# Performance work log

Measured on AMD Instinct MI355X. Metric: run time of the kernel, lower is better.

Reference implementation:

```python
import jax, jax.numpy as jnp
import numpy as np
from jax import lax

VOCAB = 32000
D_MODEL = 1024
N_LAYERS = 4
D_STATE = 8
D_CONV = 4
EXPAND = 2
D_INNER = EXPAND * D_MODEL          # 2048
DT_RANK = (D_MODEL + 15) // 16      # 64
B, L = 2, 1024


def setup_inputs() -> dict:
    key = jax.random.key(0)
    ks = jax.random.split(key, 20)
    s = 0.02
    inp = {
        "input_ids": jax.random.randint(ks[0], (B, L), 0, VOCAB, dtype=jnp.int32),
        "embed": jax.random.normal(ks[1], (VOCAB, D_MODEL), jnp.float32) * s,
        "in_proj_w": jax.random.normal(ks[2], (N_LAYERS, 2 * D_INNER, D_MODEL), jnp.float32) * s,
        "conv_w": jax.random.normal(ks[3], (N_LAYERS, D_INNER, 1, D_CONV), jnp.float32) * s,
        "conv_b": jnp.zeros((N_LAYERS, D_INNER), jnp.float32),
        "x_proj_w": jax.random.normal(ks[4], (N_LAYERS, DT_RANK + 2 * D_STATE, D_INNER), jnp.float32) * s,
        "dt_proj_w": jax.random.normal(ks[5], (N_LAYERS, D_INNER, DT_RANK), jnp.float32) * s,
        "dt_proj_b": jax.random.normal(ks[6], (N_LAYERS, D_INNER), jnp.float32) * 0.1,
        "A_log": jnp.broadcast_to(jnp.log(jnp.arange(1, D_STATE + 1, dtype=jnp.float32)),
                                  (N_LAYERS, D_INNER, D_STATE)) + 0.0,
        "D": jnp.ones((N_LAYERS, D_INNER), jnp.float32),
        "out_proj_w": jax.random.normal(ks[7], (N_LAYERS, D_MODEL, D_INNER), jnp.float32) * s,
        "ln_g": jnp.ones((N_LAYERS, D_MODEL), jnp.float32),
        "ln_b": jnp.zeros((N_LAYERS, D_MODEL), jnp.float32),
        "fn_g": jnp.ones((D_MODEL,), jnp.float32),
        "fn_b": jnp.zeros((D_MODEL,), jnp.float32),
        "fc_w": jax.random.normal(ks[8], (VOCAB, D_MODEL), jnp.float32) * s,
        "fc_b": jnp.zeros((VOCAB,), jnp.float32),
    }
    return inp


def layer_norm(x, g, b, eps=1e-5):
    mu = jnp.mean(x, -1, keepdims=True)
    var = jnp.var(x, -1, keepdims=True)
    return (x - mu) * lax.rsqrt(var + eps) * g + b


def silu(x):
    return x * jax.nn.sigmoid(x)


def selective_scan(deltaA, deltaBu, C):
    # deltaA, deltaBu: (b,l,d,n); C: (b,l,n) -> y: (b,l,d)
    def step(h, inp):
        dA, dBu, c = inp
        h = dA * h + dBu                       # (b,d,n)
        y = jnp.einsum('bdn,bn->bd', h, c)
        return h, y
    h0 = jnp.zeros(deltaA.shape[:1] + deltaA.shape[2:], deltaA.dtype)
    _, ys = lax.scan(step, h0, (deltaA.transpose(1, 0, 2, 3),
                                deltaBu.transpose(1, 0, 2, 3),
                                C.transpose(1, 0, 2)))
    return ys.transpose(1, 0, 2)


def mamba_block(x, in_proj_w, conv_w, conv_b, x_proj_w, dt_proj_w, dt_proj_b, A_log, D, out_proj_w):
    # x: (b,l,d_model)
    xz = jnp.einsum('bld,ed->ble', x, in_proj_w)          # (b,l,2*di)
    xc, z = jnp.split(xz, 2, axis=-1)
    # causal depthwise conv1d, kernel D_CONV
    xc_ncl = xc.transpose(0, 2, 1)                         # (b,di,l)
    xc_ncl = lax.conv_general_dilated(
        xc_ncl, conv_w, window_strides=(1,), padding=[(D_CONV - 1, 0)],
        feature_group_count=D_INNER, dimension_numbers=('NCH', 'OIH', 'NCH'))
    xc = silu(xc_ncl.transpose(0, 2, 1) + conv_b)          # (b,l,di)
    x_dbl = jnp.einsum('bld,ed->ble', xc, x_proj_w)        # (b,l,dt_rank+2n)
    dt, Bm, Cm = jnp.split(x_dbl, [DT_RANK, DT_RANK + D_STATE], axis=-1)
    dt = jax.nn.softplus(jnp.einsum('blr,dr->bld', dt, dt_proj_w) + dt_proj_b)  # (b,l,di)
    A = -jnp.exp(A_log)                                    # (di,n)
    deltaA = jnp.exp(dt[..., None] * A)                    # (b,l,di,n)
    deltaBu = dt[..., None] * Bm[:, :, None, :] * xc[..., None]
    y = selective_scan(deltaA, deltaBu, Cm)                # (b,l,di)
    y = y + xc * D
    y = y * silu(z)
    return jnp.einsum('ble,de->bld', y, out_proj_w)


def reference(input_ids, embed, in_proj_w, conv_w, conv_b, x_proj_w, dt_proj_w,
              dt_proj_b, A_log, D, out_proj_w, ln_g, ln_b, fn_g, fn_b, fc_w, fc_b):
    x = embed[input_ids]                                   # (b,l,d)
    for i in range(N_LAYERS):
        out = mamba_block(x, in_proj_w[i], conv_w[i], conv_b[i], x_proj_w[i],
                          dt_proj_w[i], dt_proj_b[i], A_log[i], D[i], out_proj_w[i])
        x = layer_norm(out + x, ln_g[i], ln_b[i])
    x = layer_norm(x, fn_g, fn_b)
    logits = jnp.einsum('bld,vd->blv', x, fc_w) + fc_b
    return logits
```

## Files before the change

### kernel.cpp

```cpp
#include <hip/hip_runtime.h>
#include <cstddef>
#include <cstdint>

#define D_MODEL 1024
#define D_INNER 2048
#define DT_RANK 64
#define D_STATE 8
#define NLAYERS 4
#define BATCH 2
#define SEQ 1024
#define M_ROWS (BATCH*SEQ)
#define VOCAB 32000
#define XPAD 128
#define NC 32
#define LC 32
#define XSK 8

typedef __attribute__((ext_vector_type(8))) short short8;
typedef __attribute__((ext_vector_type(4))) float f32x4;

#define GPTR(p) (const __attribute__((address_space(1))) void*)(p)
#define LPTR(p) (__attribute__((address_space(3))) void*)(p)

__device__ __forceinline__ float sigmoidf_(float x) { return 1.f / (1.f + __expf(-x)); }

__device__ __forceinline__ unsigned short f2bf(float f) {
    unsigned u = __float_as_uint(f);
    u += 0x7fffu + ((u >> 16) & 1u);
    return (unsigned short)(u >> 16);
}

__global__ __launch_bounds__(256) void cast_kernel(const float* __restrict__ in,
                                                   unsigned short* __restrict__ out, int n4)
{
    int i = blockIdx.x * 256 + threadIdx.x;
    if (i >= n4) return;
    float4 v = ((const float4*)in)[i];
    ushort4 o;
    o.x = f2bf(v.x); o.y = f2bf(v.y); o.z = f2bf(v.z); o.w = f2bf(v.w);
    ((ushort4*)out)[i] = o;
}

__global__ __launch_bounds__(256) void cast_pad_xproj(const float* __restrict__ in,
                                                      unsigned short* __restrict__ out)
{
    int i = blockIdx.x * 256 + threadIdx.x;
    if (i >= NLAYERS * XPAD * D_INNER / 4) return;
    int col4 = i & (D_INNER / 4 - 1);
    int row = (i >> 9) & (XPAD - 1);
    int layer = i >> 16;
    ushort4 o = {0, 0, 0, 0};
    if (row < 80) {
        float4 v = ((const float4*)(in + ((size_t)layer * 80 + row) * D_INNER))[col4];
        o.x = f2bf(v.x); o.y = f2bf(v.y); o.z = f2bf(v.z); o.w = f2bf(v.w);
    }
    ((ushort4*)out)[i] = o;
}

__global__ __launch_bounds__(256) void gather_kernel(const int* __restrict__ ids,
                                                     const float* __restrict__ embed,
                                                     float* __restrict__ x,
                                                     unsigned short* __restrict__ xb)
{
    int m = blockIdx.x;
    int t = threadIdx.x;
    int id = ids[m];
    float4 v = ((const float4*)(embed + (size_t)id * D_MODEL))[t];
    ((float4*)(x + (size_t)m * D_MODEL))[t] = v;
    ushort4 o;
    o.x = f2bf(v.x); o.y = f2bf(v.y); o.z = f2bf(v.z); o.w = f2bf(v.w);
    ((ushort4*)(xb + (size_t)m * D_MODEL))[t] = o;
}

template<int EPI>
__global__ __launch_bounds__(256) void gemm_bf16_nt(const unsigned short* __restrict__ A, int lda,
                                                    const unsigned short* __restrict__ B, int ldb,
                                                    float* __restrict__ C, int ldc,
                                                    int K, const float* __restrict__ bias)
{
    __shared__ unsigned short As[2][128 * 32];
    __shared__ unsigned short Bs[2][128 * 32];
    const int tid = threadIdx.x;

    const int gm = gridDim.x;
    const int bid = blockIdx.y * gm + blockIdx.x;
    const int q = (gm * gridDim.y) >> 3;
    const int swz = (bid & 7) * q + (bid >> 3);
    const int bm = (swz % gm) * 128, bn = (swz / gm) * 128;

    const int wid = tid >> 6, lane = tid & 63;
    const int wm = (wid >> 1) * 64, wn = (wid & 1) * 64;
    const int lrow = lane & 15, lkg = lane >> 4;

    const int srow = tid >> 2;
    const int ksrc = ((tid & 3) ^ ((srow >> 1) & 3)) * 8;
    const size_t kz = (size_t)blockIdx.z * K;
    const unsigned short* Ag = A + (size_t)(bm + srow) * lda + kz + ksrc;
    const unsigned short* Bg = B + (size_t)(bn + srow) * ldb + kz + ksrc;
    const size_t r64a = (size_t)64 * lda;
    const size_t r64b = (size_t)64 * ldb;

#define STAGE(buf, koff)                                                                              \
    do {                                                                                              \
        __builtin_amdgcn_global_load_lds(GPTR(Ag + (koff)),        LPTR(&As[buf][tid * 8]), 16, 0, 0);\
        __builtin_amdgcn_global_load_lds(GPTR(Ag + r64a + (koff)), LPTR(&As[buf][2048 + tid * 8]), 16, 0, 0);\
        __builtin_amdgcn_global_load_lds(GPTR(Bg + (koff)),        LPTR(&Bs[buf][tid * 8]), 16, 0, 0);\
        __builtin_amdgcn_global_load_lds(GPTR(Bg + r64b + (koff)), LPTR(&Bs[buf][2048 + tid * 8]), 16, 0, 0);\
    } while (0)

    f32x4 acc[4][4];
    #pragma unroll
    for (int i = 0; i < 4; ++i)
        #pragma unroll
        for (int j = 0; j < 4; ++j)
            acc[i][j] = f32x4{0.f, 0.f, 0.f, 0.f};

    STAGE(0, 0);
    __syncthreads();

    int cur = 0;
    for (int k0 = 0; k0 < K; k0 += 32) {
        if (k0 + 32 < K) STAGE(cur ^ 1, k0 + 32);

        short8 af[4], bf[4];
        #pragma unroll
        for (int i = 0; i < 4; ++i) {
            int ra = wm + 16 * i + lrow;
            int pa = lkg ^ ((ra >> 1) & 3);
            af[i] = *(const short8*)(&As[cur][ra * 32 + pa * 8]);
            int rb = wn + 16 * i + lrow;
            int pb = lkg ^ ((rb >> 1) & 3);
            bf[i] = *(const short8*)(&Bs[cur][rb * 32 + pb * 8]);
        }
        #pragma unroll
        for (int i = 0; i < 4; ++i)
            #pragma unroll
            for (int j = 0; j < 4; ++j)
                acc[i][j] = __builtin_amdgcn_mfma_f32_16x16x32_bf16(af[i], bf[j], acc[i][j], 0, 0, 0);

        __syncthreads();
        cur ^= 1;
    }
#undef STAGE

    if (gridDim.z > 1) C += (size_t)blockIdx.z * M_ROWS * ldc;

    const int crow = bm + wm + lkg * 4;
    const int ccol = bn + wn + lrow;
    #pragma unroll
    for (int i = 0; i < 4; ++i) {
        #pragma unroll
        for (int j = 0; j < 4; ++j) {
            float bv = (EPI == 1 || EPI == 2) ? bias[ccol + 16 * j] : 0.f;
            float* Cp = C + (size_t)(crow + 16 * i) * ldc + ccol + 16 * j;
            #pragma unroll
            for (int r = 0; r < 4; ++r) {
                float v = acc[i][j][r] + bv;
                if (EPI == 1) v = (v > 20.f) ? v : log1pf(__expf(v));
                Cp[(size_t)r * ldc] = v;
            }
        }
    }
}

__global__ __launch_bounds__(256) void reduce_xdbl(const float* __restrict__ part,
                                                   float* __restrict__ xdbl,
                                                   unsigned short* __restrict__ xdbl_b)
{
    int i = blockIdx.x * 256 + threadIdx.x;
    float4 s = ((const float4*)part)[i];
    #pragma unroll
    for (int z = 1; z < XSK; ++z) {
        float4 v = ((const float4*)part)[(size_t)z * (M_ROWS * XPAD / 4) + i];
        s.x += v.x; s.y += v.y; s.z += v.z; s.w += v.w;
    }
    ((float4*)xdbl)[i] = s;
    ushort4 o;
    o.x = f2bf(s.x); o.y = f2bf(s.y); o.z = f2bf(s.z); o.w = f2bf(s.w);
    ((ushort4*)xdbl_b)[i] = o;
}

__global__ __launch_bounds__(256) void conv_silu_kernel(const float* __restrict__ xz,
                                                        const float* __restrict__ cw,
                                                        const float* __restrict__ cb,
                                                        float* __restrict__ xc,
                                                        unsigned short* __restrict__ xcb)
{
    int idx = blockIdx.x * 256 + threadIdx.x;
    int d = idx & (D_INNER - 1);
    int m = idx >> 11;
    int l = m & (SEQ - 1);
    int b = m >> 10;
    float w0 = cw[d * 4 + 0], w1 = cw[d * 4 + 1], w2 = cw[d * 4 + 2], w3 = cw[d * 4 + 3];
    float s = cb[d];
    const float* base = xz + ((size_t)b * SEQ) * (2 * D_INNER) + d;
    if (l - 3 >= 0) s += base[(size_t)(l - 3) * (2 * D_INNER)] * w0;
    if (l - 2 >= 0) s += base[(size_t)(l - 2) * (2 * D_INNER)] * w1;
    if (l - 1 >= 0) s += base[(size_t)(l - 1) * (2 * D_INNER)] * w2;
    s += base[(size_t)l * (2 * D_INNER)] * w3;
    float v = s * sigmoidf_(s);
    xc[(size_t)m * D_INNER + d] = v;
    xcb[(size_t)m * D_INNER + d] = f2bf(v);
}

__global__ __launch_bounds__(256) void scan_partial(const float* __restrict__ dt,
                                                    const float* __restrict__ xdbl,
                                                    const float* __restrict__ xc,
                                                    const float* __restrict__ A_log,
                                                    float* __restrict__ H,
                                                    float* __restrict__ P)
{
    const int tid = threadIdx.x;
    const int b = blockIdx.x & 1;
    const int c = (blockIdx.x >> 1) & (NC - 1);
    const int d = ((blockIdx.x >> 6) << 8) + tid;

    __shared__ float Bs[LC][8];
    {
        int r = tid >> 3, n = tid & 7;
        Bs[r][n] = xdbl[(size_t)(b * SEQ + c * LC + r) * XPAD + DT_RANK + n];
    }
    __syncthreads();

    float An[8];
    #pragma unroll
    for (int n = 0; n < 8; ++n) An[n] = -__expf(A_log[d * 8 + n]);
    float h[8] = {0.f,0.f,0.f,0.f,0.f,0.f,0.f,0.f};
    float p[8] = {1.f,1.f,1.f,1.f,1.f,1.f,1.f,1.f};

    const float* dtp = dt + (size_t)(b * SEQ + c * LC) * D_INNER + d;
    const float* xcp = xc + (size_t)(b * SEQ + c * LC) * D_INNER + d;
    for (int l = 0; l < LC; ++l) {
        float dtv = dtp[(size_t)l * D_INNER];
        float ux  = dtv * xcp[(size_t)l * D_INNER];
        #pragma unroll
        for (int n = 0; n < 8; ++n) {
            float dA = __expf(dtv * An[n]);
            h[n] = dA * h[n] + Bs[l][n] * ux;
            p[n] *= dA;
        }
    }
    size_t base = (size_t)((b * NC + c) * 8) * D_INNER + d;
    #pragma unroll
    for (int n = 0; n < 8; ++n) {
        H[base + (size_t)n * D_INNER] = h[n];
        P[base + (size_t)n * D_INNER] = p[n];
    }
}

__global__ __launch_bounds__(256) void scan_combine(const float* __restrict__ H,
                                                    float* __restrict__ P )
{
    int idx = blockIdx.x * 256 + threadIdx.x;
    int d = idx & (D_INNER - 1);
    int n = (idx >> 11) & 7;
    int b = idx >> 14;
    float hp = 0.f;
    for (int c = 0; c < NC; ++c) {
        size_t base = (size_t)((b * NC + c) * 8 + n) * D_INNER + d;
        float Pv = P[base], Hv = H[base];
        P[base] = hp;
        hp = Pv * hp + Hv;
    }
}

__global__ __launch_bounds__(256) void scan_final(const float* __restrict__ dt,
                                                  const float* __restrict__ xdbl,
                                                  const float* __restrict__ xc,
                                                  const float* __restrict__ xz,
                                                  const float* __restrict__ A_log,
                                                  const float* __restrict__ Dp,
                                                  const float* __restrict__ h0,
                                                  unsigned short* __restrict__ yb)
{
    const int tid = threadIdx.x;
    const int b = blockIdx.x & 1;
    const int c = (blockIdx.x >> 1) & (NC - 1);
    const int d = ((blockIdx.x >> 6) << 8) + tid;

    __shared__ float Bs[LC][8];
    __shared__ float Cs[LC][8];
    {
        int r = tid >> 3, n = tid & 7;
        size_t xrow = (size_t)(b * SEQ + c * LC + r) * XPAD;
        Bs[r][n] = xdbl[xrow + DT_RANK + n];
        Cs[r][n] = xdbl[xrow + DT_RANK + 8 + n];
    }
    __syncthreads();

    float An[8], h[8];
    size_t base = (size_t)((b * NC + c) * 8) * D_INNER + d;
    #pragma unroll
    for (int n = 0; n < 8; ++n) {
        An[n] = -__expf(A_log[d * 8 + n]);
        h[n] = h0[base + (size_t)n * D_INNER];
    }
    const float Dv = Dp[d];

    const float* dtp = dt + (size_t)(b * SEQ + c * LC) * D_INNER + d;
    const float* xcp = xc + (size_t)(b * SEQ + c * LC) * D_INNER + d;
    const float* zp  = xz + (size_t)(b * SEQ + c * LC) * (2 * D_INNER) + D_INNER + d;
    unsigned short* ybp = yb + (size_t)(b * SEQ + c * LC) * D_INNER + d;

    for (int l = 0; l < LC; ++l) {
        float dtv = dtp[(size_t)l * D_INNER];
        float xcv = xcp[(size_t)l * D_INNER];
        float zv  = zp[(size_t)l * (2 * D_INNER)];
        float ux = dtv * xcv;
        float acc = 0.f;
        #pragma unroll
        for (int n = 0; n < 8; ++n) {
            float dA = __expf(dtv * An[n]);
            h[n] = dA * h[n] + Bs[l][n] * ux;
            acc += h[n] * Cs[l][n];
        }
        float yv = (acc + xcv * Dv) * (zv * sigmoidf_(zv));
        ybp[(size_t)l * D_INNER] = f2bf(yv);
    }
}

template<bool ADD>
__global__ __launch_bounds__(256) void ln_kernel(const float* __restrict__ extra,
                                                 const float* __restrict__ xin,
                                                 float* __restrict__ xout,
                                                 unsigned short* __restrict__ xbout,
                                                 const float* __restrict__ g,
                                                 const float* __restrict__ bb)
{
    int m = blockIdx.x;
    int t = threadIdx.x;
    float4 v = ((const float4*)(xin + (size_t)m * D_MODEL))[t];
    if (ADD) {
        float4 e = ((const float4*)(extra + (size_t)m * D_MODEL))[t];
        v.x += e.x; v.y += e.y; v.z += e.z; v.w += e.w;
    }
    float s  = v.x + v.y + v.z + v.w;
    float s2 = v.x * v.x + v.y * v.y + v.z * v.z + v.w * v.w;
    for (int off = 32; off; off >>= 1) {
        s  += __shfl_down(s, off);
        s2 += __shfl_down(s2, off);
    }
    __shared__ float red[8];
    int wid = t >> 6, lane = t & 63;
    if (lane == 0) { red[wid] = s; red[wid + 4] = s2; }
    __syncthreads();
    if (t == 0) {
        float a  = red[0] + red[1] + red[2] + red[3];
        float b2 = red[4] + red[5] + red[6] + red[7];
        float mu = a * (1.f / D_MODEL);
        red[0] = mu;
        red[4] = b2 * (1.f / D_MODEL) - mu * mu;
    }
    __syncthreads();
    float mu = red[0];
    float rs = rsqrtf(red[4] + 1e-5f);
    float4 gg = ((const float4*)g)[t];
    float4 bv = ((const float4*)bb)[t];
    float4 o;
    o.x = (v.x - mu) * rs * gg.x + bv.x;
    o.y = (v.y - mu) * rs * gg.y + bv.y;
    o.z = (v.z - mu) * rs * gg.z + bv.z;
    o.w = (v.w - mu) * rs * gg.w + bv.w;
    ((float4*)(xout + (size_t)m * D_MODEL))[t] = o;
    ushort4 ob;
    ob.x = f2bf(o.x); ob.y = f2bf(o.y); ob.z = f2bf(o.z); ob.w = f2bf(o.w);
    ((ushort4*)(xbout + (size_t)m * D_MODEL))[t] = ob;
}

extern "C" void kernel_launch(void* const* d_in, const int* in_sizes, int n_in,
                              void* d_out, int out_size, void* d_ws, size_t ws_size,
                              hipStream_t stream)
{
    const int*   ids      = (const int*)d_in[0];
    const float* embed    = (const float*)d_in[1];
    const float* in_proj  = (const float*)d_in[2];
    const float* conv_w   = (const float*)d_in[3];
    const float* conv_b   = (const float*)d_in[4];
    const float* x_proj   = (const float*)d_in[5];
    const float* dt_w     = (const float*)d_in[6];
    const float* dt_b     = (const float*)d_in[7];
    const float* A_log    = (const float*)d_in[8];
    const float* Dp       = (const float*)d_in[9];
    const float* out_proj = (const float*)d_in[10];
    const float* ln_g     = (const float*)d_in[11];
    const float* ln_b     = (const float*)d_in[12];
    const float* fn_g     = (const float*)d_in[13];
    const float* fn_b     = (const float*)d_in[14];
    const float* fc_w     = (const float*)d_in[15];
    const float* fc_b     = (const float*)d_in[16];
    float* logits = (float*)d_out;

    float* ws = (float*)d_ws;
    float* x     = ws;
    float* xz    = x + (size_t)M_ROWS * D_MODEL;
    float* xc    = xz + (size_t)M_ROWS * 2 * D_INNER;
    float* xdbl  = xc + (size_t)M_ROWS * D_INNER;
    float* dtbuf = xdbl + (size_t)M_ROWS * XPAD;
    float* tmp   = dtbuf + (size_t)M_ROWS * D_INNER;
    float* xpart = tmp + (size_t)M_ROWS * D_MODEL;

    float* Hbuf = tmp;
    float* Pbuf = tmp + (size_t)BATCH * NC * D_STATE * D_INNER;

    unsigned short* xb     = (unsigned short*)(xpart + (size_t)XSK * M_ROWS * XPAD);
    unsigned short* yb     = xb + (size_t)M_ROWS * D_MODEL;
    unsigned short* xcb    = yb + (size_t)M_ROWS * D_INNER;
    unsigned short* xdbl_b = xcb + (size_t)M_ROWS * D_INNER;
    unsigned short* wb_in  = xdbl_b + (size_t)M_ROWS * XPAD;
    unsigned short* wb_out = wb_in + (size_t)NLAYERS * 2 * D_INNER * D_MODEL;
    unsigned short* wb_fc  = wb_out + (size_t)NLAYERS * D_MODEL * D_INNER;
    unsigned short* wb_x   = wb_fc + (size_t)VOCAB * D_MODEL;
    unsigned short* wb_dt  = wb_x + (size_t)NLAYERS * XPAD * D_INNER;

    {
        int n4 = NLAYERS * 2 * D_INNER * D_MODEL / 4;
        cast_kernel<<<(n4 + 255) / 256, 256, 0, stream>>>(in_proj, wb_in, n4);
        n4 = NLAYERS * D_MODEL * D_INNER / 4;
        cast_kernel<<<(n4 + 255) / 256, 256, 0, stream>>>(out_proj, wb_out, n4);
        n4 = VOCAB * D_MODEL / 4;
        cast_kernel<<<(n4 + 255) / 256, 256, 0, stream>>>(fc_w, wb_fc, n4);
        n4 = NLAYERS * D_INNER * DT_RANK / 4;
        cast_kernel<<<(n4 + 255) / 256, 256, 0, stream>>>(dt_w, wb_dt, n4);
        n4 = NLAYERS * XPAD * D_INNER / 4;
        cast_pad_xproj<<<(n4 + 255) / 256, 256, 0, stream>>>(x_proj, wb_x);
    }

    gather_kernel<<<M_ROWS, 256, 0, stream>>>(ids, embed, x, xb);

    for (int i = 0; i < NLAYERS; ++i) {
        const unsigned short* W_in_b  = wb_in + (size_t)i * 2 * D_INNER * D_MODEL;
        const unsigned short* W_out_b = wb_out + (size_t)i * D_MODEL * D_INNER;
        const unsigned short* W_x_b   = wb_x + (size_t)i * XPAD * D_INNER;
        const unsigned short* W_dt_b  = wb_dt + (size_t)i * D_INNER * DT_RANK;
        const float* cw    = conv_w + (size_t)i * D_INNER * 4;
        const float* cb    = conv_b + (size_t)i * D_INNER;
        const float* b_dt  = dt_b + (size_t)i * D_INNER;
        const float* Al    = A_log + (size_t)i * D_INNER * D_STATE;
        const float* Dl    = Dp + (size_t)i * D_INNER;
        const float* g     = ln_g + (size_t)i * D_MODEL;
        const float* bb    = ln_b + (size_t)i * D_MODEL;

        gemm_bf16_nt<0><<<dim3(M_ROWS / 128, 2 * D_INNER / 128), 256, 0, stream>>>(
            xb, D_MODEL, W_in_b, D_MODEL, xz, 2 * D_INNER, D_MODEL, nullptr);

        conv_silu_kernel<<<(M_ROWS * D_INNER) / 256, 256, 0, stream>>>(xz, cw, cb, xc, xcb);

        gemm_bf16_nt<0><<<dim3(M_ROWS / 128, 1, XSK), 256, 0, stream>>>(
            xcb, D_INNER, W_x_b, D_INNER, xpart, XPAD, D_INNER / XSK, nullptr);
        reduce_xdbl<<<(M_ROWS * XPAD / 4) / 256, 256, 0, stream>>>(xpart, xdbl, xdbl_b);

        gemm_bf16_nt<1><<<dim3(M_ROWS / 128, D_INNER / 128), 256, 0, stream>>>(
            xdbl_b, XPAD, W_dt_b, DT_RANK, dtbuf, D_INNER, DT_RANK, b_dt);

        scan_partial<<<BATCH * NC * (D_INNER / 256), 256, 0, stream>>>(
            dtbuf, xdbl, xc, Al, Hbuf, Pbuf);
        scan_combine<<<(BATCH * D_STATE * D_INNER) / 256, 256, 0, stream>>>(Hbuf, Pbuf);
        scan_final<<<BATCH * NC * (D_INNER / 256), 256, 0, stream>>>(
            dtbuf, xdbl, xc, xz, Al, Dl, Pbuf, yb);

        gemm_bf16_nt<0><<<dim3(M_ROWS / 128, D_MODEL / 128), 256, 0, stream>>>(
            yb, D_INNER, W_out_b, D_INNER, tmp, D_MODEL, D_INNER, nullptr);

        ln_kernel<true><<<M_ROWS, 256, 0, stream>>>(tmp, x, x, xb, g, bb);
    }

    ln_kernel<false><<<M_ROWS, 256, 0, stream>>>(nullptr, x, tmp, xb, fn_g, fn_b);

    gemm_bf16_nt<2><<<dim3(M_ROWS / 128, VOCAB / 128), 256, 0, stream>>>(
        xb, D_MODEL, wb_fc, D_MODEL, logits, VOCAB, D_MODEL, fc_b);
}
```

Measured before the change: 1.017 ms.

## Use 256x256 tile GEMM for vocab projection and relax pipeline barrier waits

Adds a 512-thread GEMM kernel with 256x256 output tiles, used for the final vocab logits projection, to raise arithmetic intensity and cut operand reloads. The existing 128x128 GEMM and the new one now use explicit vmcnt waits plus raw s_barrier instead of __syncthreads. This lets the next stage's async global-to-LDS loads stay in flight during compute. The larger tile uses more accumulator registers and LDS, which can lower occupancy. The grid also has fewer blocks along N (VOCAB/256 = 125).

```diff
diff --git a/kernel.cpp b/kernel.cpp
--- a/kernel.cpp
+++ b/kernel.cpp
@@ -116,11 +116,17 @@
             acc[i][j] = f32x4{0.f, 0.f, 0.f, 0.f};
 
     STAGE(0, 0);
-    __syncthreads();
 
     int cur = 0;
     for (int k0 = 0; k0 < K; k0 += 32) {
-        if (k0 + 32 < K) STAGE(cur ^ 1, k0 + 32);
+        if (k0 + 32 < K) {
+            STAGE(cur ^ 1, k0 + 32);
+            asm volatile("s_waitcnt vmcnt(4)" ::: "memory");
+        } else {
+            asm volatile("s_waitcnt vmcnt(0)" ::: "memory");
+        }
+        __builtin_amdgcn_s_barrier();
+        __builtin_amdgcn_sched_barrier(0);
 
         short8 af[4], bf[4];
         #pragma unroll
@@ -138,7 +144,7 @@
             for (int j = 0; j < 4; ++j)
                 acc[i][j] = __builtin_amdgcn_mfma_f32_16x16x32_bf16(af[i], bf[j], acc[i][j], 0, 0, 0);
 
-        __syncthreads();
+        __builtin_amdgcn_s_barrier();
         cur ^= 1;
     }
 #undef STAGE
@@ -159,6 +165,100 @@
                 if (EPI == 1) v = (v > 20.f) ? v : log1pf(__expf(v));
                 Cp[(size_t)r * ldc] = v;
             }
+        }
+    }
+}
+
+template<int EPI>
+__global__ __launch_bounds__(512) void gemm_bf16_nt256(const unsigned short* __restrict__ A, int lda,
+                                                       const unsigned short* __restrict__ B, int ldb,
+                                                       float* __restrict__ C, int ldc,
+                                                       int K, const float* __restrict__ bias)
+{
+    __shared__ unsigned short As[2][256 * 32];
+    __shared__ unsigned short Bs[2][256 * 32];
+    const int tid = threadIdx.x;
+
+    const int gm = gridDim.x;
+    const int bid = blockIdx.y * gm + blockIdx.x;
+    const int q = (gm * gridDim.y) >> 3;
+    const int swz = (bid & 7) * q + (bid >> 3);
+    const int bm = (swz % gm) * 256, bn = (swz / gm) * 256;
+
+    const int wid = tid >> 6, lane = tid & 63;
+    const int wm = (wid >> 2) * 128, wn = (wid & 3) * 64;
+    const int lrow = lane & 15, lkg = lane >> 4;
+
+    const int srow = tid >> 2;
+    const int ksrc = ((tid & 3) ^ ((srow >> 1) & 3)) * 8;
+    const unsigned short* Ag = A + (size_t)(bm + srow) * lda + ksrc;
+    const unsigned short* Bg = B + (size_t)(bn + srow) * ldb + ksrc;
+    const size_t r128a = (size_t)128 * lda;
+    const size_t r128b = (size_t)128 * ldb;
+
+#define STAGE2(buf, koff)                                                                               \
+    do {                                                                                                \
+        __builtin_amdgcn_global_load_lds(GPTR(Ag + (koff)),         LPTR(&As[buf][tid * 8]), 16, 0, 0); \
+        __builtin_amdgcn_global_load_lds(GPTR(Ag + r128a + (koff)), LPTR(&As[buf][4096 + tid * 8]), 16, 0, 0);\
+        __builtin_amdgcn_global_load_lds(GPTR(Bg + (koff)),         LPTR(&Bs[buf][tid * 8]), 16, 0, 0); \
+        __builtin_amdgcn_global_load_lds(GPTR(Bg + r128b + (koff)), LPTR(&Bs[buf][4096 + tid * 8]), 16, 0, 0);\
+    } while (0)
+
+    f32x4 acc[8][4];
+    #pragma unroll
+    for (int i = 0; i < 8; ++i)
+        #pragma unroll
+        for (int j = 0; j < 4; ++j)
+            acc[i][j] = f32x4{0.f, 0.f, 0.f, 0.f};
+
+    STAGE2(0, 0);
+
+    int cur = 0;
+    for (int k0 = 0; k0 < K; k0 += 32) {
+        if (k0 + 32 < K) {
+            STAGE2(cur ^ 1, k0 + 32);
+            asm volatile("s_waitcnt vmcnt(4)" ::: "memory");
+        } else {
+            asm volatile("s_waitcnt vmcnt(0)" ::: "memory");
+        }
+        __builtin_amdgcn_s_barrier();
+        __builtin_amdgcn_sched_barrier(0);
+
+        short8 af[8], bf[4];
+        #pragma unroll
+        for (int j = 0; j < 4; ++j) {
+            int rb = wn + 16 * j + lrow;
+            int pb = lkg ^ ((rb >> 1) & 3);
+            bf[j] = *(const short8*)(&Bs[cur][rb * 32 + pb * 8]);
+        }
+        #pragma unroll
+        for (int i = 0; i < 8; ++i) {
+            int ra = wm + 16 * i + lrow;
+            int pa = lkg ^ ((ra >> 1) & 3);
+            af[i] = *(const short8*)(&As[cur][ra * 32 + pa * 8]);
+        }
+        #pragma unroll
+        for (int i = 0; i < 8; ++i)
+            #pragma unroll
+            for (int j = 0; j < 4; ++j)
+                acc[i][j] = __builtin_amdgcn_mfma_f32_16x16x32_bf16(af[i], bf[j], acc[i][j], 0, 0, 0);
+
+        __builtin_amdgcn_s_barrier();
+        cur ^= 1;
+    }
+#undef STAGE2
+
+    const int crow = bm + wm + lkg * 4;
+    const int ccol = bn + wn + lrow;
+    #pragma unroll
+    for (int i = 0; i < 8; ++i) {
+        #pragma unroll
+        for (int j = 0; j < 4; ++j) {
+            float bv = (EPI == 2) ? bias[ccol + 16 * j] : 0.f;
+            float* Cp = C + (size_t)(crow + 16 * i) * ldc + ccol + 16 * j;
+            #pragma unroll
+            for (int r = 0; r < 4; ++r)
+                Cp[(size_t)r * ldc] = acc[i][j][r] + bv;
         }
     }
 }
@@ -466,6 +566,6 @@
 
     ln_kernel<false><<<M_ROWS, 256, 0, stream>>>(nullptr, x, tmp, xb, fn_g, fn_b);
 
-    gemm_bf16_nt<2><<<dim3(M_ROWS / 128, VOCAB / 128), 256, 0, stream>>>(
+    gemm_bf16_nt256<2><<<dim3(M_ROWS / 256, VOCAB / 256), 512, 0, stream>>>(
         xb, D_MODEL, wb_fc, D_MODEL, logits, VOCAB, D_MODEL, fc_b);
 }
```

Result: no change. 1.001 ms (-1.6%).
